# Kernel tuning notes

Hardware: AMD Instinct MI355X
Metric: run time of the kernel (lower is better)

Reference implementation:

```python
import jax, jax.numpy as jnp
import numpy as np

OBS, H, F1, A, T, B = 128, 128, 256, 18, 128, 1024


def _ln(x, w, b, eps=1e-5):
    mu = jnp.mean(x, -1, keepdims=True)
    xc = x - mu
    var = jnp.mean(xc * xc, -1, keepdims=True)
    return xc * jax.lax.rsqrt(var + eps) * w + b


def _features(x, w1, b1, w2, b2, lnw, lnb):
    h = jax.nn.relu(x @ w1.T + b1)      # [N, 256]
    h = h @ w2.T + b2                   # [N, 128]
    return jax.nn.relu(_ln(h, lnw, lnb))


def _masked_lstm(xs, ds, h0, c0, wih, whh, b):
    # xs: [T,B,H], ds: [T,B] float; PyTorch gate order i,f,g,o
    def step(carry, inp):
        h, c = carry
        xt, dt = inp
        m = (1.0 - dt)[:, None]
        h = h * m
        c = c * m
        g = xt @ wih.T + h @ whh.T + b  # [B, 4H]
        i, f, gg, o = jnp.split(g, 4, axis=-1)
        c = jax.nn.sigmoid(f) * c + jax.nn.sigmoid(i) * jnp.tanh(gg)
        h = jax.nn.sigmoid(o) * jnp.tanh(c)
        return (h, c), h
    (hT, cT), hs = jax.lax.scan(step, (h0, c0), (xs, ds))
    return hs, hT, cT


def setup_inputs() -> dict:
    key = jax.random.key(0)
    ks = iter(jax.random.split(key, 64))
    p = lambda shape, s=0.05: jax.random.normal(next(ks), shape, jnp.float32) * s
    inp = {
        'x': jax.random.normal(next(ks), (T * B, OBS), jnp.float32),
        'actor_h': jnp.zeros((1, B, H), jnp.float32),
        'actor_c': jnp.zeros((1, B, H), jnp.float32),
        'critic_h': jnp.zeros((1, B, H), jnp.float32),
        'critic_c': jnp.zeros((1, B, H), jnp.float32),
        'done': jax.random.randint(next(ks), (T * B,), 0, 2, jnp.int32),
        'action': jax.random.randint(next(ks), (T * B,), 0, A, jnp.int64),
        # actor params
        'af_w1': p((F1, OBS)), 'af_b1': p((F1,)),
        'af_w2': p((H, F1)), 'af_b2': p((H,)),
        'af_lnw': jnp.ones((H,), jnp.float32), 'af_lnb': jnp.zeros((H,), jnp.float32),
        'a_wih': p((4 * H, H)), 'a_whh': p((4 * H, H)), 'a_b': p((4 * H,)),
        'a_lnw': jnp.ones((H,), jnp.float32), 'a_lnb': jnp.zeros((H,), jnp.float32),
        'a_hw': p((A, H)), 'a_hb': p((A,)),
        # critic params
        'cf_w1': p((F1, OBS)), 'cf_b1': p((F1,)),
        'cf_w2': p((H, F1)), 'cf_b2': p((H,)),
        'cf_lnw': jnp.ones((H,), jnp.float32), 'cf_lnb': jnp.zeros((H,), jnp.float32),
        'c_wih': p((4 * H, H)), 'c_whh': p((4 * H, H)), 'c_b': p((4 * H,)),
        'c_lnw': jnp.ones((H,), jnp.float32), 'c_lnb': jnp.zeros((H,), jnp.float32),
        'c_hw': p((1, H)), 'c_hb': p((1,)),
    }
    return inp


def reference(x, actor_h, actor_c, critic_h, critic_c,
              af_w1, af_b1, af_w2, af_b2, af_lnw, af_lnb,
              a_wih, a_whh, a_b, a_lnw, a_lnb, a_hw, a_hb,
              cf_w1, cf_b1, cf_w2, cf_b2, cf_lnw, cf_lnb,
              c_wih, c_whh, c_b, c_lnw, c_lnb, c_hw, c_hb,
              done, action):
    bsz = actor_h.shape[1]
    ds = done.astype(jnp.float32).reshape(-1, bsz)  # [T, B]

    # actor branch
    af = _features(x, af_w1, af_b1, af_w2, af_b2, af_lnw, af_lnb).reshape(-1, bsz, H)
    hs, ahT, acT = _masked_lstm(af, ds, actor_h[0], actor_c[0], a_wih, a_whh, a_b)
    ah = _ln(hs.reshape(-1, H), a_lnw, a_lnb)
    logits = ah @ a_hw.T + a_hb                     # [N, A]
    logp_all = jax.nn.log_softmax(logits)
    logp = jnp.take_along_axis(logp_all, action[:, None], axis=1)[:, 0]
    entropy = -jnp.sum(jnp.exp(logp_all) * logp_all, axis=-1)

    # critic branch
    cf = _features(x, cf_w1, cf_b1, cf_w2, cf_b2, cf_lnw, cf_lnb).reshape(-1, bsz, H)
    cs, chT, ccT = _masked_lstm(cf, ds, critic_h[0], critic_c[0], c_wih, c_whh, c_b)
    ch = _ln(cs.reshape(-1, H), c_lnw, c_lnb)
    value = ch @ c_hw.T + c_hb                      # [N, 1]

    return (action, logp, entropy, value,
            ahT[None], acT[None], chT[None], ccT[None])
```

## Files before the change

### kernel.cpp

```cpp
#include <hip/hip_runtime.h>
#include <stdint.h>
#include <stddef.h>

#define OBS 128
#define F1D 256
#define HD  128
#define NA  18
#define TT  128
#define BB  1024
#define NN  (TT*BB)

typedef __attribute__((ext_vector_type(8))) short short8;
typedef __attribute__((ext_vector_type(4))) float f32x4;

#define WS_W1   0u
#define WS_W2   131072u
#define WS_WC   262144u
#define WS_FLAG 786432u
#define WS_FEAT 787456u

__device__ __forceinline__ unsigned short f2bf(float f) {
  union { float f; uint32_t u; } v; v.f = f;
  uint32_t u = v.u;
  u += 0x7fffu + ((u >> 16) & 1u);
  return (unsigned short)(u >> 16);
}
__device__ __forceinline__ float bf2f(uint32_t hu) {
  union { uint32_t u; float f; } v; v.u = hu << 16;
  return v.f;
}
__device__ __forceinline__ float fsigm(float x) {
  float e = __builtin_amdgcn_exp2f(-1.442695041f * x);
  return __builtin_amdgcn_rcpf(1.0f + e);
}
__device__ __forceinline__ float ftanh(float x) {
  float e = __builtin_amdgcn_exp2f(-2.885390082f * x);
  return __builtin_fmaf(2.0f, __builtin_amdgcn_rcpf(1.0f + e), -1.0f);
}
__device__ __forceinline__ f32x4 mfma16(short8 a, short8 b, f32x4 c) {
  return __builtin_amdgcn_mfma_f32_16x16x32_bf16(a, b, c, 0, 0, 0);
}

__global__ __launch_bounds__(256) void prep_kernel(
    const float* __restrict__ aw1, const float* __restrict__ cw1,
    const float* __restrict__ aw2, const float* __restrict__ cw2,
    const float* __restrict__ awih, const float* __restrict__ awhh,
    const float* __restrict__ cwih, const float* __restrict__ cwhh,
    const int* __restrict__ action,
    unsigned short* __restrict__ w1o, unsigned short* __restrict__ w2o,
    unsigned short* __restrict__ wco, int* __restrict__ flag)
{
  int bid = blockIdx.x;
  if (bid == (int)gridDim.x - 1) {
    __shared__ int any;
    if (threadIdx.x == 0) any = 0;
    __syncthreads();
    int local = 0;
    for (int i = threadIdx.x; i < 4096; i += 256)
      if ((i & 1) && action[i] != 0) local = 1;
    if (local) any = 1;
    __syncthreads();
    if (threadIdx.x == 0) flag[0] = any;
    return;
  }
  int i = bid * 256 + threadIdx.x;
  if (i < 65536) {
    int br = i >> 15, j = i & 32767;
    const float* s = br ? cw1 : aw1;
    w1o[i] = f2bf(s[j]);
  } else if (i < 131072) {
    int k = i - 65536;
    int br = k >> 15, j = k & 32767;
    const float* s = br ? cw2 : aw2;
    w2o[k] = f2bf(s[j]);
  } else {
    int k = i - 131072;
    int br = k >> 17, j = k & 131071;
    int n = j >> 8, kk = j & 255;
    const float* wih = br ? cwih : awih;
    const float* whh = br ? cwhh : awhh;
    float v = (kk < 128) ? wih[n*128 + kk] : whh[n*128 + (kk - 128)];
    wco[k] = f2bf(v);
  }
}

__global__ __launch_bounds__(512, 2) void feat_kernel(
    const float* __restrict__ x,
    const unsigned short* __restrict__ w1g, const unsigned short* __restrict__ w2g,
    const float* __restrict__ ab1, const float* __restrict__ cb1,
    const float* __restrict__ ab2, const float* __restrict__ cb2,
    const float* __restrict__ alnw, const float* __restrict__ clnw,
    const float* __restrict__ alnb, const float* __restrict__ clnb,
    unsigned short* __restrict__ featg)
{
  int br = blockIdx.y;
  const unsigned short* w1 = w1g + (size_t)br * (F1D*OBS);
  const unsigned short* w2 = w2g + (size_t)br * (HD*F1D);
  const float* b1 = br ? cb1 : ab1;
  const float* b2 = br ? cb2 : ab2;
  const float* lw = br ? clnw : alnw;
  const float* lb = br ? clnb : alnb;
  unsigned short* feat = featg + (size_t)br * NN * HD;

  __shared__ unsigned short xs[32*128];
  __shared__ unsigned short h1s[32*256];
  __shared__ float fs[32*140];
  __shared__ float lws[HD], lbs[HD];

  int tid = threadIdx.x;
  int w = tid >> 6, lane = tid & 63, q = lane >> 4, ln = lane & 15;

  short8 b1f[2][4]; float b1v[2];
  for (int ct = 0; ct < 2; ++ct) {
    int nn = w*32 + ct*16 + ln;
    b1v[ct] = b1[nn];
    for (int kf = 0; kf < 4; ++kf)
      b1f[ct][kf] = *(const short8*)&w1[nn*OBS + kf*32 + q*8];
  }
  short8 b2f[8]; float b2v;
  int nn2 = w*16 + ln;
  b2v = b2[nn2];
  for (int kf = 0; kf < 8; ++kf)
    b2f[kf] = *(const short8*)&w2[nn2*F1D + kf*32 + q*8];
  if (tid < HD) { lws[tid] = lw[tid]; lbs[tid] = lb[tid]; }

  for (int it = 0; it < 4; ++it) {
    int row0 = blockIdx.x * 128 + it * 32;
    const float* xp = x + (size_t)row0 * OBS;
    for (int s = 0; s < 2; ++s) {
      int e4 = tid + s*512;
      int e  = e4 * 4;
      int r  = e >> 7, k = e & 127;
      float4 v = ((const float4*)xp)[e4];
      int sw = ((k >> 3) ^ (r & 15)) << 3;
      int ad = r*128 + sw + (k & 7);
      *(uint32_t*)&xs[ad]     = (uint32_t)f2bf(v.x) | ((uint32_t)f2bf(v.y) << 16);
      *(uint32_t*)&xs[ad + 2] = (uint32_t)f2bf(v.z) | ((uint32_t)f2bf(v.w) << 16);
    }
    __syncthreads();
    for (int mt = 0; mt < 2; ++mt) {
      short8 af[4];
      for (int kf = 0; kf < 4; ++kf)
        af[kf] = *(const short8*)&xs[(mt*16 + ln)*128 + ((((kf<<2)|q) ^ ln) << 3)];
      for (int ct = 0; ct < 2; ++ct) {
        f32x4 acc = {b1v[ct], b1v[ct], b1v[ct], b1v[ct]};
        for (int kf = 0; kf < 4; ++kf) acc = mfma16(af[kf], b1f[ct][kf], acc);
        int nn = w*32 + ct*16 + ln;
        for (int rg = 0; rg < 4; ++rg) {
          float v = acc[rg] > 0.0f ? acc[rg] : 0.0f;
          int rrow = mt*16 + q*4 + rg;
          int sw = ((nn >> 3) ^ (rrow & 15)) << 3;
          h1s[rrow*256 + sw + (nn & 7)] = f2bf(v);
        }
      }
    }
    __syncthreads();
    for (int mt = 0; mt < 2; ++mt) {
      short8 ah[8];
      for (int kf = 0; kf < 8; ++kf)
        ah[kf] = *(const short8*)&h1s[(mt*16 + ln)*256 + ((((kf<<2)|q) ^ ln) << 3)];
      f32x4 acc = {b2v, b2v, b2v, b2v};
      for (int kf = 0; kf < 8; ++kf) acc = mfma16(ah[kf], b2f[kf], acc);
      for (int rg = 0; rg < 4; ++rg)
        fs[(mt*16 + q*4 + rg)*140 + nn2] = acc[rg];
    }
    __syncthreads();
    {
      int r = tid >> 4, g = tid & 15;
      float4 v0 = *(const float4*)&fs[r*140 + g*8];
      float4 v1 = *(const float4*)&fs[r*140 + g*8 + 4];
      float s  = v0.x+v0.y+v0.z+v0.w + v1.x+v1.y+v1.z+v1.w;
      float ss = v0.x*v0.x+v0.y*v0.y+v0.z*v0.z+v0.w*v0.w
               + v1.x*v1.x+v1.y*v1.y+v1.z*v1.z+v1.w*v1.w;
      for (int m = 1; m < 16; m <<= 1) { s += __shfl_xor(s, m); ss += __shfl_xor(ss, m); }
      float mu = s * (1.0f/128.0f);
      float var = ss * (1.0f/128.0f) - mu*mu;
      float rstd = rsqrtf(var + 1e-5f);
      float vv[8] = {v0.x,v0.y,v0.z,v0.w,v1.x,v1.y,v1.z,v1.w};
      unsigned short ob[8];
      for (int j = 0; j < 8; ++j) {
        int k = g*8 + j;
        float t = (vv[j] - mu) * rstd * lws[k] + lbs[k];
        ob[j] = f2bf(t > 0.0f ? t : 0.0f);
      }
      *(short8*)&feat[(size_t)(row0 + r)*HD + g*8] = *(short8*)ob;
    }
    __syncthreads();
  }
}

__global__ __launch_bounds__(512, 2) void lstm_kernel(
    const unsigned short* __restrict__ wcg,
    const float* __restrict__ ab, const float* __restrict__ cb,
    const float* __restrict__ ah0, const float* __restrict__ ac0,
    const float* __restrict__ ch0, const float* __restrict__ cc0,
    const int* __restrict__ done,
    unsigned short* __restrict__ featg,
    float* __restrict__ dout)
{
  int bid = blockIdx.x;
  int br = bid >> 6;
  int base = (bid & 63) * 16;
  const unsigned short* wc = wcg + (size_t)br * (512*256);
  const float* bias_g = br ? cb : ab;
  const float* h0 = br ? ch0 : ah0;
  const float* c0 = br ? cc0 : ac0;
  unsigned short* hsbuf = featg + (size_t)br * NN * HD;
  float* outh = dout + (size_t)(4 + br*2) * NN;
  float* outc = dout + (size_t)(5 + br*2) * NN;

  int tid = threadIdx.x;
  int w = tid >> 6, lane = tid & 63, q = lane >> 4, ln = lane & 15;
  int n = w*16 + ln;

  short8 bfr[4][8];
  float bias[4];
  for (int g4 = 0; g4 < 4; ++g4) {
    int gn = g4*128 + n;
    bias[g4] = bias_g[gn];
    for (int kf = 0; kf < 8; ++kf)
      bfr[g4][kf] = *(const short8*)&wc[gn*256 + kf*32 + q*8];
  }

  __shared__ float mls[TT*16];
  __shared__ unsigned short hlds[2][16*128];
  for (int i = tid; i < TT*16; i += 512)
    mls[i] = 1.0f - (float)done[(i >> 4)*BB + base + (i & 15)];

  float hp[4], cp[4], h0v[4];
  for (int rg = 0; rg < 4; ++rg) {
    int r = q*4 + rg;
    h0v[rg] = h0[(base + r)*HD + n];
    cp[rg]  = c0[(base + r)*HD + n];
    hp[rg]  = h0v[rg];
  }
  short8 afr[4];
  {
    const unsigned short* fp = hsbuf + ((size_t)(base + ln))*HD;
    for (int kf = 0; kf < 4; ++kf)
      afr[kf] = *(const short8*)&fp[kf*32 + q*8];
  }
  __syncthreads();
  {
    float4 m0 = *(const float4*)&mls[q*4];
    for (int rg = 0; rg < 4; ++rg) {
      float m = (&m0.x)[rg];
      cp[rg] *= m;
      int r = q*4 + rg;
      hlds[0][r*128 + (((n >> 3) ^ r) << 3) + (n & 7)] = f2bf(h0v[rg] * m);
    }
  }
  __syncthreads();

  for (int t = 0; t < TT; ++t) {
    const unsigned short* hb = hlds[t & 1];
    unsigned short* hbn = hlds[(t & 1) ^ 1];
    short8 hfr[4];
    for (int kf = 0; kf < 4; ++kf)
      hfr[kf] = *(const short8*)&hb[ln*128 + ((((kf<<2)|q) ^ ln) << 3)];
    int tn = (t < TT-1) ? t + 1 : TT-1;
    short8 nfr[4];
    {
      const unsigned short* fp = hsbuf + ((size_t)(tn*BB + base + ln))*HD;
      for (int kf = 0; kf < 4; ++kf)
        nfr[kf] = *(const short8*)&fp[kf*32 + q*8];
    }
    f32x4 a0 = {bias[0],bias[0],bias[0],bias[0]};
    f32x4 a1 = {bias[1],bias[1],bias[1],bias[1]};
    f32x4 a2 = {bias[2],bias[2],bias[2],bias[2]};
    f32x4 a3 = {bias[3],bias[3],bias[3],bias[3]};
    for (int kf = 0; kf < 4; ++kf) {
      a0 = mfma16(afr[kf], bfr[0][kf], a0);
      a1 = mfma16(afr[kf], bfr[1][kf], a1);
      a2 = mfma16(afr[kf], bfr[2][kf], a2);
      a3 = mfma16(afr[kf], bfr[3][kf], a3);
    }
    for (int kf = 0; kf < 4; ++kf) {
      a0 = mfma16(hfr[kf], bfr[0][4+kf], a0);
      a1 = mfma16(hfr[kf], bfr[1][4+kf], a1);
      a2 = mfma16(hfr[kf], bfr[2][4+kf], a2);
      a3 = mfma16(hfr[kf], bfr[3][4+kf], a3);
    }
    float4 mn;
    if (t < TT-1) mn = *(const float4*)&mls[(t+1)*16 + q*4];
    else          mn = make_float4(1.0f, 1.0f, 1.0f, 1.0f);
    for (int rg = 0; rg < 4; ++rg) {
      float si = fsigm(a0[rg]);
      float sf = fsigm(a1[rg]);
      float tg = ftanh(a2[rg]);
      float so = fsigm(a3[rg]);
      float cn = sf*cp[rg] + si*tg;
      float hn = so*ftanh(cn);
      hsbuf[((size_t)(t*BB + base + q*4 + rg))*HD + n] = f2bf(hn);
      float m = (&mn.x)[rg];
      cp[rg] = cn * m;
      hp[rg] = hn;
      int r = q*4 + rg;
      hbn[r*128 + (((n >> 3) ^ r) << 3) + (n & 7)] = f2bf(hn * m);
    }
    __syncthreads();
    for (int kf = 0; kf < 4; ++kf) afr[kf] = nfr[kf];
  }
  for (int rg = 0; rg < 4; ++rg) {
    int r = base + q*4 + rg;
    outh[r*HD + n] = hp[rg];
    outc[r*HD + n] = cp[rg];
  }
}

__global__ __launch_bounds__(256) void head_kernel(
    const unsigned short* __restrict__ hsa, const unsigned short* __restrict__ hsc,
    const float* __restrict__ alnw, const float* __restrict__ alnb,
    const float* __restrict__ ahw, const float* __restrict__ ahb,
    const float* __restrict__ clnw, const float* __restrict__ clnb,
    const float* __restrict__ chw, const float* __restrict__ chb,
    const int* __restrict__ action, const int* __restrict__ flag,
    float* __restrict__ dout)
{
  __shared__ float whs[NA*HD];
  __shared__ float hbs[NA];
  __shared__ float alws[HD], albs[HD], clws[HD], clbs[HD], cws[HD];
  __shared__ float cbs;
  int tid = threadIdx.x;
  for (int i = tid; i < NA*HD; i += 256) whs[i] = ahw[i];
  if (tid < NA) hbs[tid] = ahb[tid];
  if (tid < HD) { alws[tid]=alnw[tid]; albs[tid]=alnb[tid];
                  clws[tid]=clnw[tid]; clbs[tid]=clnb[tid]; cws[tid]=chw[tid]; }
  if (tid == 0) cbs = chb[0];
  __syncthreads();

  int rr = blockIdx.x*256 + tid;
  int fl = flag[0];
  int act = fl ? action[rr] : (int)(((const long long*)action)[rr]);
  dout[rr] = (float)act;
  if (act < 0) act = 0;
  if (act > NA-1) act = NA-1;

  uint32_t hw_[64];
  {
    const uint32_t* hp = (const uint32_t*)(hsa + (size_t)rr*HD);
    for (int i = 0; i < 16; ++i) *(uint4*)&hw_[i*4] = ((const uint4*)hp)[i];
    float s = 0.0f, ss = 0.0f;
    for (int i = 0; i < 64; ++i) {
      float f0 = bf2f(hw_[i] & 0xffffu), f1 = bf2f(hw_[i] >> 16);
      s += f0 + f1; ss += f0*f0 + f1*f1;
    }
    float mu = s * (1.0f/128.0f);
    float var = ss * (1.0f/128.0f) - mu*mu;
    float rstd = rsqrtf(var + 1e-5f);
    float lg[NA];
    for (int a = 0; a < NA; ++a) lg[a] = hbs[a];
    for (int i = 0; i < 64; ++i) {
      int k0 = i*2;
      float f0 = (bf2f(hw_[i] & 0xffffu) - mu)*rstd*alws[k0]   + albs[k0];
      float f1 = (bf2f(hw_[i] >> 16)     - mu)*rstd*alws[k0+1] + albs[k0+1];
      for (int a = 0; a < NA; ++a)
        lg[a] += f0*whs[a*HD + k0] + f1*whs[a*HD + k0 + 1];
    }
    float mx = lg[0];
    for (int a = 1; a < NA; ++a) mx = fmaxf(mx, lg[a]);
    float se = 0.0f;
    for (int a = 0; a < NA; ++a) se += __expf(lg[a] - mx);
    float lse = __logf(se);
    dout[(size_t)NN + rr] = lg[act] - mx - lse;
    float ent = 0.0f;
    for (int a = 0; a < NA; ++a) { float lp = lg[a] - mx - lse; ent -= __expf(lp)*lp; }
    dout[(size_t)2*NN + rr] = ent;
  }
  {
    const uint32_t* hp = (const uint32_t*)(hsc + (size_t)rr*HD);
    for (int i = 0; i < 16; ++i) *(uint4*)&hw_[i*4] = ((const uint4*)hp)[i];
    float s = 0.0f, ss = 0.0f;
    for (int i = 0; i < 64; ++i) {
      float f0 = bf2f(hw_[i] & 0xffffu), f1 = bf2f(hw_[i] >> 16);
      s += f0 + f1; ss += f0*f0 + f1*f1;
    }
    float mu = s * (1.0f/128.0f);
    float var = ss * (1.0f/128.0f) - mu*mu;
    float rstd = rsqrtf(var + 1e-5f);
    float v = cbs;
    for (int i = 0; i < 64; ++i) {
      int k0 = i*2;
      float f0 = (bf2f(hw_[i] & 0xffffu) - mu)*rstd*clws[k0]   + clbs[k0];
      float f1 = (bf2f(hw_[i] >> 16)     - mu)*rstd*clws[k0+1] + clbs[k0+1];
      v += f0*cws[k0] + f1*cws[k0+1];
    }
    dout[(size_t)3*NN + rr] = v;
  }
}

extern "C" void kernel_launch(void* const* d_in, const int* in_sizes, int n_in,
                              void* d_out, int out_size, void* d_ws, size_t ws_size,
                              hipStream_t stream) {
  (void)in_sizes; (void)n_in; (void)out_size; (void)ws_size;
  const float* x    = (const float*)d_in[0];
  const float* ah0  = (const float*)d_in[1];
  const float* ac0  = (const float*)d_in[2];
  const float* ch0  = (const float*)d_in[3];
  const float* cc0  = (const float*)d_in[4];
  const int*   done = (const int*)d_in[5];
  const int*   act  = (const int*)d_in[6];
  const float* aw1  = (const float*)d_in[7];
  const float* ab1  = (const float*)d_in[8];
  const float* aw2  = (const float*)d_in[9];
  const float* ab2  = (const float*)d_in[10];
  const float* aflnw= (const float*)d_in[11];
  const float* aflnb= (const float*)d_in[12];
  const float* awih = (const float*)d_in[13];
  const float* awhh = (const float*)d_in[14];
  const float* a_b  = (const float*)d_in[15];
  const float* alnw = (const float*)d_in[16];
  const float* alnb = (const float*)d_in[17];
  const float* ahw  = (const float*)d_in[18];
  const float* ahb  = (const float*)d_in[19];
  const float* cw1  = (const float*)d_in[20];
  const float* cb1  = (const float*)d_in[21];
  const float* cw2  = (const float*)d_in[22];
  const float* cb2  = (const float*)d_in[23];
  const float* cflnw= (const float*)d_in[24];
  const float* cflnb= (const float*)d_in[25];
  const float* cwih = (const float*)d_in[26];
  const float* cwhh = (const float*)d_in[27];
  const float* c_b  = (const float*)d_in[28];
  const float* clnw = (const float*)d_in[29];
  const float* clnb = (const float*)d_in[30];
  const float* chw  = (const float*)d_in[31];
  const float* chb  = (const float*)d_in[32];

  char* ws = (char*)d_ws;
  unsigned short* w1b  = (unsigned short*)(ws + WS_W1);
  unsigned short* w2b  = (unsigned short*)(ws + WS_W2);
  unsigned short* wcb  = (unsigned short*)(ws + WS_WC);
  int*            flag = (int*)(ws + WS_FLAG);
  unsigned short* featb= (unsigned short*)(ws + WS_FEAT);
  unsigned short* hsa  = featb;
  unsigned short* hsc  = featb + (size_t)NN * HD;
  float* out = (float*)d_out;

  prep_kernel<<<1537, 256, 0, stream>>>(aw1, cw1, aw2, cw2, awih, awhh, cwih, cwhh,
                                        act, w1b, w2b, wcb, flag);
  feat_kernel<<<dim3(NN/128, 2), 512, 0, stream>>>(x, w1b, w2b, ab1, cb1, ab2, cb2,
                                                   aflnw, cflnw, aflnb, cflnb, featb);
  lstm_kernel<<<128, 512, 0, stream>>>(wcb, a_b, c_b, ah0, ac0, ch0, cc0, done,
                                       featb, out);
  head_kernel<<<512, 256, 0, stream>>>(hsa, hsc, alnw, alnb, ahw, ahb,
                                       clnw, clnb, chw, chb, act, flag, out);
}
```

Baseline: 513.4 us.

## Prescale LSTM gate weights for exp2, restructure feature kernel to 32-row blocks

Folds the -log2e (and -2log2e for the cell gate) scaling into the bf16 LSTM weights and a precomputed bias table, so the sequential recurrence can call exp2 directly without a multiply. Replaces the mask multiply with a select and uses a lighter barrier in the recurrence loop, plus pointer-increment addressing. The feature kernel is changed from 512-thread blocks looping over 128 rows to 256-thread blocks that each handle 32 rows, with weights loaded per tile instead of kept in registers. This trades weight reuse in the feature kernel for more blocks and lower register pressure. Applying the gate scale before bf16 rounding slightly changes numerics.

After: 542.3 us. 1.06x slower.

```diff
diff --git a/kernel.cpp b/kernel.cpp
--- a/kernel.cpp
+++ b/kernel.cpp
@@ -17,7 +17,10 @@
 #define WS_W2   131072u
 #define WS_WC   262144u
 #define WS_FLAG 786432u
-#define WS_FEAT 787456u
+#define WS_BIAS 787456u
+#define WS_FEAT 791552u
+
+#define LOG2E 1.442695041f
 
 __device__ __forceinline__ unsigned short f2bf(float f) {
   union { float f; uint32_t u; } v; v.f = f;
@@ -29,16 +32,16 @@
   union { uint32_t u; float f; } v; v.u = hu << 16;
   return v.f;
 }
-__device__ __forceinline__ float fsigm(float x) {
-  float e = __builtin_amdgcn_exp2f(-1.442695041f * x);
-  return __builtin_amdgcn_rcpf(1.0f + e);
-}
-__device__ __forceinline__ float ftanh(float x) {
-  float e = __builtin_amdgcn_exp2f(-2.885390082f * x);
-  return __builtin_fmaf(2.0f, __builtin_amdgcn_rcpf(1.0f + e), -1.0f);
-}
 __device__ __forceinline__ f32x4 mfma16(short8 a, short8 b, f32x4 c) {
   return __builtin_amdgcn_mfma_f32_16x16x32_bf16(a, b, c, 0, 0, 0);
+}
+__device__ __forceinline__ short8 ldg128(const unsigned short* p) {
+  int4 r;
+  asm volatile("global_load_dwordx4 %0, %1, off" : "=v"(r) : "v"(p));
+  return *(short8*)&r;
+}
+__device__ __forceinline__ void wg_barrier() {
+  asm volatile("s_waitcnt lgkmcnt(0)\n\ts_barrier" ::: "memory");
 }
 
 __global__ __launch_bounds__(256) void prep_kernel(
@@ -46,9 +49,11 @@
     const float* __restrict__ aw2, const float* __restrict__ cw2,
     const float* __restrict__ awih, const float* __restrict__ awhh,
     const float* __restrict__ cwih, const float* __restrict__ cwhh,
+    const float* __restrict__ a_b, const float* __restrict__ c_b,
     const int* __restrict__ action,
     unsigned short* __restrict__ w1o, unsigned short* __restrict__ w2o,
-    unsigned short* __restrict__ wco, int* __restrict__ flag)
+    unsigned short* __restrict__ wco, float* __restrict__ sbias,
+    int* __restrict__ flag)
 {
   int bid = blockIdx.x;
   if (bid == (int)gridDim.x - 1) {
@@ -61,6 +66,12 @@
     if (local) any = 1;
     __syncthreads();
     if (threadIdx.x == 0) flag[0] = any;
+    for (int j = threadIdx.x; j < 1024; j += 256) {
+      int br = j >> 9, idx = j & 511;
+      const float* src = br ? c_b : a_b;
+      float sc = ((idx >> 7) == 2) ? -2.0f*LOG2E : -LOG2E;
+      sbias[j] = src[idx] * sc;
+    }
     return;
   }
   int i = bid * 256 + threadIdx.x;
@@ -80,11 +91,12 @@
     const float* wih = br ? cwih : awih;
     const float* whh = br ? cwhh : awhh;
     float v = (kk < 128) ? wih[n*128 + kk] : whh[n*128 + (kk - 128)];
-    wco[k] = f2bf(v);
-  }
-}
-
-__global__ __launch_bounds__(512, 2) void feat_kernel(
+    float sc = ((n >> 7) == 2) ? -2.0f*LOG2E : -LOG2E;
+    wco[k] = f2bf(v * sc);
+  }
+}
+
+__global__ __launch_bounds__(256) void feat_kernel(
     const float* __restrict__ x,
     const unsigned short* __restrict__ w1g, const unsigned short* __restrict__ w2g,
     const float* __restrict__ ab1, const float* __restrict__ cb1,
@@ -101,97 +113,119 @@
   const float* lw = br ? clnw : alnw;
   const float* lb = br ? clnb : alnb;
   unsigned short* feat = featg + (size_t)br * NN * HD;
+  int row0 = blockIdx.x * 32;
 
   __shared__ unsigned short xs[32*128];
   __shared__ unsigned short h1s[32*256];
-  __shared__ float fs[32*140];
+  __shared__ float fs[32*132];
   __shared__ float lws[HD], lbs[HD];
 
   int tid = threadIdx.x;
   int w = tid >> 6, lane = tid & 63, q = lane >> 4, ln = lane & 15;
 
-  short8 b1f[2][4]; float b1v[2];
-  for (int ct = 0; ct < 2; ++ct) {
-    int nn = w*32 + ct*16 + ln;
-    b1v[ct] = b1[nn];
+  const float* xp = x + (size_t)row0 * OBS;
+  #pragma unroll
+  for (int s = 0; s < 4; ++s) {
+    int e4 = tid + s*256;
+    int e  = e4 * 4;
+    int r  = e >> 7, k = e & 127;
+    float4 v = ((const float4*)xp)[e4];
+    int sw = ((k >> 3) ^ (r & 15)) << 3;
+    int ad = r*128 + sw + (k & 7);
+    *(uint32_t*)&xs[ad]     = (uint32_t)f2bf(v.x) | ((uint32_t)f2bf(v.y) << 16);
+    *(uint32_t*)&xs[ad + 2] = (uint32_t)f2bf(v.z) | ((uint32_t)f2bf(v.w) << 16);
+  }
+  if (tid < HD) { lws[tid] = lw[tid]; lbs[tid] = lb[tid]; }
+  __syncthreads();
+
+  short8 af[2][4];
+  #pragma unroll
+  for (int mt = 0; mt < 2; ++mt)
+    #pragma unroll
     for (int kf = 0; kf < 4; ++kf)
-      b1f[ct][kf] = *(const short8*)&w1[nn*OBS + kf*32 + q*8];
-  }
-  short8 b2f[8]; float b2v;
-  int nn2 = w*16 + ln;
-  b2v = b2[nn2];
-  for (int kf = 0; kf < 8; ++kf)
-    b2f[kf] = *(const short8*)&w2[nn2*F1D + kf*32 + q*8];
-  if (tid < HD) { lws[tid] = lw[tid]; lbs[tid] = lb[tid]; }
-
-  for (int it = 0; it < 4; ++it) {
-    int row0 = blockIdx.x * 128 + it * 32;
-    const float* xp = x + (size_t)row0 * OBS;
-    for (int s = 0; s < 2; ++s) {
-      int e4 = tid + s*512;
-      int e  = e4 * 4;
-      int r  = e >> 7, k = e & 127;
-      float4 v = ((const float4*)xp)[e4];
-      int sw = ((k >> 3) ^ (r & 15)) << 3;
-      int ad = r*128 + sw + (k & 7);
-      *(uint32_t*)&xs[ad]     = (uint32_t)f2bf(v.x) | ((uint32_t)f2bf(v.y) << 16);
-      *(uint32_t*)&xs[ad + 2] = (uint32_t)f2bf(v.z) | ((uint32_t)f2bf(v.w) << 16);
-    }
-    __syncthreads();
+      af[mt][kf] = *(const short8*)&xs[(mt*16 + ln)*128 + ((((kf<<2)|q) ^ ln) << 3)];
+  #pragma unroll
+  for (int ct = 0; ct < 4; ++ct) {
+    int nn = w*64 + ct*16 + ln;
+    float bv = b1[nn];
+    short8 bf[4];
+    #pragma unroll
+    for (int kf = 0; kf < 4; ++kf)
+      bf[kf] = *(const short8*)&w1[nn*OBS + kf*32 + q*8];
+    #pragma unroll
     for (int mt = 0; mt < 2; ++mt) {
-      short8 af[4];
-      for (int kf = 0; kf < 4; ++kf)
-        af[kf] = *(const short8*)&xs[(mt*16 + ln)*128 + ((((kf<<2)|q) ^ ln) << 3)];
-      for (int ct = 0; ct < 2; ++ct) {
-        f32x4 acc = {b1v[ct], b1v[ct], b1v[ct], b1v[ct]};
-        for (int kf = 0; kf < 4; ++kf) acc = mfma16(af[kf], b1f[ct][kf], acc);
-        int nn = w*32 + ct*16 + ln;
-        for (int rg = 0; rg < 4; ++rg) {
-          float v = acc[rg] > 0.0f ? acc[rg] : 0.0f;
-          int rrow = mt*16 + q*4 + rg;
-          int sw = ((nn >> 3) ^ (rrow & 15)) << 3;
-          h1s[rrow*256 + sw + (nn & 7)] = f2bf(v);
-        }
+      f32x4 acc = {bv, bv, bv, bv};
+      #pragma unroll
+      for (int kf = 0; kf < 4; ++kf) acc = mfma16(af[mt][kf], bf[kf], acc);
+      #pragma unroll
+      for (int rg = 0; rg < 4; ++rg) {
+        float v = acc[rg] > 0.0f ? acc[rg] : 0.0f;
+        int rrow = mt*16 + q*4 + rg;
+        int sw = ((nn >> 3) ^ (rrow & 15)) << 3;
+        h1s[rrow*256 + sw + (nn & 7)] = f2bf(v);
       }
     }
-    __syncthreads();
+  }
+  __syncthreads();
+
+  short8 ah[2][8];
+  #pragma unroll
+  for (int mt = 0; mt < 2; ++mt)
+    #pragma unroll
+    for (int kf = 0; kf < 8; ++kf)
+      ah[mt][kf] = *(const short8*)&h1s[(mt*16 + ln)*256 + ((((kf<<2)|q) ^ ln) << 3)];
+  #pragma unroll
+  for (int nt = 0; nt < 2; ++nt) {
+    int nn = w*32 + nt*16 + ln;
+    float bv = b2[nn];
+    short8 bf[8];
+    #pragma unroll
+    for (int kf = 0; kf < 8; ++kf)
+      bf[kf] = *(const short8*)&w2[nn*F1D + kf*32 + q*8];
+    #pragma unroll
     for (int mt = 0; mt < 2; ++mt) {
-      short8 ah[8];
-      for (int kf = 0; kf < 8; ++kf)
-        ah[kf] = *(const short8*)&h1s[(mt*16 + ln)*256 + ((((kf<<2)|q) ^ ln) << 3)];
-      f32x4 acc = {b2v, b2v, b2v, b2v};
-      for (int kf = 0; kf < 8; ++kf) acc = mfma16(ah[kf], b2f[kf], acc);
+      f32x4 acc = {bv, bv, bv, bv};
+      #pragma unroll
+      for (int kf = 0; kf < 8; ++kf) acc = mfma16(ah[mt][kf], bf[kf], acc);
+      #pragma unroll
       for (int rg = 0; rg < 4; ++rg)
-        fs[(mt*16 + q*4 + rg)*140 + nn2] = acc[rg];
-    }
-    __syncthreads();
-    {
-      int r = tid >> 4, g = tid & 15;
-      float4 v0 = *(const float4*)&fs[r*140 + g*8];
-      float4 v1 = *(const float4*)&fs[r*140 + g*8 + 4];
-      float s  = v0.x+v0.y+v0.z+v0.w + v1.x+v1.y+v1.z+v1.w;
-      float ss = v0.x*v0.x+v0.y*v0.y+v0.z*v0.z+v0.w*v0.w
-               + v1.x*v1.x+v1.y*v1.y+v1.z*v1.z+v1.w*v1.w;
-      for (int m = 1; m < 16; m <<= 1) { s += __shfl_xor(s, m); ss += __shfl_xor(ss, m); }
-      float mu = s * (1.0f/128.0f);
-      float var = ss * (1.0f/128.0f) - mu*mu;
-      float rstd = rsqrtf(var + 1e-5f);
-      float vv[8] = {v0.x,v0.y,v0.z,v0.w,v1.x,v1.y,v1.z,v1.w};
-      unsigned short ob[8];
-      for (int j = 0; j < 8; ++j) {
-        int k = g*8 + j;
-        float t = (vv[j] - mu) * rstd * lws[k] + lbs[k];
-        ob[j] = f2bf(t > 0.0f ? t : 0.0f);
-      }
-      *(short8*)&feat[(size_t)(row0 + r)*HD + g*8] = *(short8*)ob;
-    }
-    __syncthreads();
+        fs[(mt*16 + q*4 + rg)*132 + nn] = acc[rg];
+    }
+  }
+  __syncthreads();
+
+  {
+    int r = tid >> 3, g = tid & 7;
+    float v[16];
+    float s = 0.0f, ss = 0.0f;
+    #pragma unroll
+    for (int j4 = 0; j4 < 4; ++j4) {
+      float4 vv = *(const float4*)&fs[r*132 + g*16 + j4*4];
+      v[j4*4+0] = vv.x; v[j4*4+1] = vv.y; v[j4*4+2] = vv.z; v[j4*4+3] = vv.w;
+      s += vv.x + vv.y + vv.z + vv.w;
+      ss += vv.x*vv.x + vv.y*vv.y + vv.z*vv.z + vv.w*vv.w;
+    }
+    #pragma unroll
+    for (int m = 1; m < 8; m <<= 1) { s += __shfl_xor(s, m); ss += __shfl_xor(ss, m); }
+    float mu = s * (1.0f/128.0f);
+    float var = ss * (1.0f/128.0f) - mu*mu;
+    float rstd = rsqrtf(var + 1e-5f);
+    unsigned short ob[16];
+    #pragma unroll
+    for (int j = 0; j < 16; ++j) {
+      int k = g*16 + j;
+      float t = (v[j] - mu) * rstd * lws[k] + lbs[k];
+      ob[j] = f2bf(t > 0.0f ? t : 0.0f);
+    }
+    unsigned short* dst = &feat[(size_t)(row0 + r)*HD + g*16];
+    *(short8*)dst       = *(short8*)&ob[0];
+    *(short8*)(dst + 8) = *(short8*)&ob[8];
   }
 }
 
 __global__ __launch_bounds__(512, 2) void lstm_kernel(
     const unsigned short* __restrict__ wcg,
-    const float* __restrict__ ab, const float* __restrict__ cb,
+    const float* __restrict__ sbias,
     const float* __restrict__ ah0, const float* __restrict__ ac0,
     const float* __restrict__ ch0, const float* __restrict__ cc0,
     const int* __restrict__ done,
@@ -202,7 +236,7 @@
   int br = bid >> 6;
   int base = (bid & 63) * 16;
   const unsigned short* wc = wcg + (size_t)br * (512*256);
-  const float* bias_g = br ? cb : ab;
+  const float* sb = sbias + br*512;
   const float* h0 = br ? ch0 : ah0;
   const float* c0 = br ? cc0 : ac0;
   unsigned short* hsbuf = featg + (size_t)br * NN * HD;
@@ -215,12 +249,15 @@
 
   short8 bfr[4][8];
   float bias[4];
+  #pragma unroll
   for (int g4 = 0; g4 < 4; ++g4) {
     int gn = g4*128 + n;
-    bias[g4] = bias_g[gn];
+    bias[g4] = sb[gn];
+    #pragma unroll
     for (int kf = 0; kf < 8; ++kf)
-      bfr[g4][kf] = *(const short8*)&wc[gn*256 + kf*32 + q*8];
-  }
+      bfr[g4][kf] = ldg128(&wc[gn*256 + kf*32 + q*8]);
+  }
+  asm volatile("s_waitcnt vmcnt(0)" ::: "memory");
 
   __shared__ float mls[TT*16];
   __shared__ unsigned short hlds[2][16*128];
@@ -228,21 +265,23 @@
     mls[i] = 1.0f - (float)done[(i >> 4)*BB + base + (i & 15)];
 
   float hp[4], cp[4], h0v[4];
+  #pragma unroll
   for (int rg = 0; rg < 4; ++rg) {
     int r = q*4 + rg;
     h0v[rg] = h0[(base + r)*HD + n];
     cp[rg]  = c0[(base + r)*HD + n];
     hp[rg]  = h0v[rg];
   }
+  const unsigned short* fp = hsbuf + ((size_t)(base + ln))*HD;
   short8 afr[4];
-  {
-    const unsigned short* fp = hsbuf + ((size_t)(base + ln))*HD;
-    for (int kf = 0; kf < 4; ++kf)
-      afr[kf] = *(const short8*)&fp[kf*32 + q*8];
-  }
+  #pragma unroll
+  for (int kf = 0; kf < 4; ++kf)
+    afr[kf] = *(const short8*)&fp[kf*32 + q*8];
+  unsigned short* sp = hsbuf + (size_t)(base + q*4)*HD + n;
   __syncthreads();
   {
     float4 m0 = *(const float4*)&mls[q*4];
+    #pragma unroll
     for (int rg = 0; rg < 4; ++rg) {
       float m = (&m0.x)[rg];
       cp[rg] *= m;
@@ -256,12 +295,13 @@
     const unsigned short* hb = hlds[t & 1];
     unsigned short* hbn = hlds[(t & 1) ^ 1];
     short8 hfr[4];
+    #pragma unroll
     for (int kf = 0; kf < 4; ++kf)
       hfr[kf] = *(const short8*)&hb[ln*128 + ((((kf<<2)|q) ^ ln) << 3)];
-    int tn = (t < TT-1) ? t + 1 : TT-1;
+    fp += (size_t)BB * HD;
     short8 nfr[4];
-    {
-      const unsigned short* fp = hsbuf + ((size_t)(tn*BB + base + ln))*HD;
+    if (t < TT-1) {
+      #pragma unroll
       for (int kf = 0; kf < 4; ++kf)
         nfr[kf] = *(const short8*)&fp[kf*32 + q*8];
     }
@@ -269,12 +309,14 @@
     f32x4 a1 = {bias[1],bias[1],bias[1],bias[1]};
     f32x4 a2 = {bias[2],bias[2],bias[2],bias[2]};
     f32x4 a3 = {bias[3],bias[3],bias[3],bias[3]};
+    #pragma unroll
     for (int kf = 0; kf < 4; ++kf) {
       a0 = mfma16(afr[kf], bfr[0][kf], a0);
       a1 = mfma16(afr[kf], bfr[1][kf], a1);
       a2 = mfma16(afr[kf], bfr[2][kf], a2);
       a3 = mfma16(afr[kf], bfr[3][kf], a3);
     }
+    #pragma unroll
     for (int kf = 0; kf < 4; ++kf) {
       a0 = mfma16(hfr[kf], bfr[0][4+kf], a0);
       a1 = mfma16(hfr[kf], bfr[1][4+kf], a1);
@@ -284,23 +326,31 @@
     float4 mn;
     if (t < TT-1) mn = *(const float4*)&mls[(t+1)*16 + q*4];
     else          mn = make_float4(1.0f, 1.0f, 1.0f, 1.0f);
+    #pragma unroll
     for (int rg = 0; rg < 4; ++rg) {
-      float si = fsigm(a0[rg]);
-      float sf = fsigm(a1[rg]);
-      float tg = ftanh(a2[rg]);
-      float so = fsigm(a3[rg]);
-      float cn = sf*cp[rg] + si*tg;
-      float hn = so*ftanh(cn);
-      hsbuf[((size_t)(t*BB + base + q*4 + rg))*HD + n] = f2bf(hn);
-      float m = (&mn.x)[rg];
-      cp[rg] = cn * m;
+      float si = __builtin_amdgcn_rcpf(1.0f + __builtin_amdgcn_exp2f(a0[rg]));
+      float sf = __builtin_amdgcn_rcpf(1.0f + __builtin_amdgcn_exp2f(a1[rg]));
+      float tg = __builtin_fmaf(2.0f,
+                   __builtin_amdgcn_rcpf(1.0f + __builtin_amdgcn_exp2f(a2[rg])), -1.0f);
+      float so = __builtin_amdgcn_rcpf(1.0f + __builtin_amdgcn_exp2f(a3[rg]));
+      float cn = __builtin_fmaf(sf, cp[rg], si*tg);
+      float th = __builtin_fmaf(2.0f,
+                   __builtin_amdgcn_rcpf(1.0f + __builtin_amdgcn_exp2f(-2.0f*LOG2E*cn)), -1.0f);
+      float hn = so * th;
+      unsigned short hu = f2bf(hn);
+      sp[rg*HD] = hu;
+      bool live = ((&mn.x)[rg] != 0.0f);
+      cp[rg] = live ? cn : 0.0f;
       hp[rg] = hn;
       int r = q*4 + rg;
-      hbn[r*128 + (((n >> 3) ^ r) << 3) + (n & 7)] = f2bf(hn * m);
-    }
-    __syncthreads();
+      hbn[r*128 + (((n >> 3) ^ r) << 3) + (n & 7)] = live ? hu : (unsigned short)0;
+    }
+    sp += (size_t)BB * HD;
+    wg_barrier();
+    #pragma unroll
     for (int kf = 0; kf < 4; ++kf) afr[kf] = nfr[kf];
   }
+  #pragma unroll
   for (int rg = 0; rg < 4; ++rg) {
     int r = base + q*4 + rg;
     outh[r*HD + n] = hp[rg];
@@ -432,16 +482,17 @@
   unsigned short* w2b  = (unsigned short*)(ws + WS_W2);
   unsigned short* wcb  = (unsigned short*)(ws + WS_WC);
   int*            flag = (int*)(ws + WS_FLAG);
+  float*          sb   = (float*)(ws + WS_BIAS);
   unsigned short* featb= (unsigned short*)(ws + WS_FEAT);
   unsigned short* hsa  = featb;
   unsigned short* hsc  = featb + (size_t)NN * HD;
   float* out = (float*)d_out;
 
   prep_kernel<<<1537, 256, 0, stream>>>(aw1, cw1, aw2, cw2, awih, awhh, cwih, cwhh,
-                                        act, w1b, w2b, wcb, flag);
-  feat_kernel<<<dim3(NN/128, 2), 512, 0, stream>>>(x, w1b, w2b, ab1, cb1, ab2, cb2,
-                                                   aflnw, cflnw, aflnb, cflnb, featb);
-  lstm_kernel<<<128, 512, 0, stream>>>(wcb, a_b, c_b, ah0, ac0, ch0, cc0, done,
+                                        a_b, c_b, act, w1b, w2b, wcb, sb, flag);
+  feat_kernel<<<dim3(NN/32, 2), 256, 0, stream>>>(x, w1b, w2b, ab1, cb1, ab2, cb2,
+                                                  aflnw, cflnw, aflnb, cflnb, featb);
+  lstm_kernel<<<128, 512, 0, stream>>>(wcb, sb, ah0, ac0, ch0, cc0, done,
                                        featb, out);
   head_kernel<<<512, 256, 0, stream>>>(hsa, hsc, alnw, alnb, ahw, ahb,
                                        clnw, clnb, chw, chb, act, flag, out);
```
